# Kernel optimization log

Hardware: AMD Instinct MI355X
Metric: run time of the kernel (lower is better)

Reference implementation:

```python
import jax, jax.numpy as jnp
import numpy as np

B, L, H, NH = 4, 1024, 768, 12      # docs, seq len, hidden, attn heads
E, M, P = 30, 8, 512                # entities/doc, mentions/entity, ht pairs/doc
NLAB = 97                           # DocRED relation count
EMB, BLK = 768, 64                  # emb_size, block_size
OFFSET = 1                          # bert cls offset


def setup_inputs() -> dict:
    key = jax.random.key(0)
    ks = jax.random.split(key, 24)
    def n(k, shp, s=0.02):
        return jax.random.normal(k, shp, jnp.float32) * s
    seq_out = jax.random.normal(ks[0], (B, L, H), jnp.float32)
    attn = jax.random.uniform(ks[1], (B, NH, L, L), jnp.float32)
    mention_idx = jax.random.randint(ks[2], (B, E, M), 0, L - 2)
    ht_pairs = jax.random.randint(ks[3], (B, P, 2), 0, E)
    label_emb = jax.random.normal(ks[4], (NLAB, H), jnp.float32)
    adj = (jax.random.uniform(ks[5], (NLAB, NLAB)) < 0.2).astype(jnp.int32)
    label_adj = jnp.maximum(adj, jnp.eye(NLAB, dtype=jnp.int32))  # self loops
    return dict(
        seq_out=seq_out, attn=attn, mention_idx=mention_idx, ht_pairs=ht_pairs,
        label_adj=label_adj, label_emb=label_emb,
        gW0=n(ks[6], (H, 2 * 500)), gal0=n(ks[7], (2, 500)), gar0=n(ks[8], (2, 500)),
        gW1=n(ks[9], (1000, 2 * 500)), gal1=n(ks[10], (2, 500)), gar1=n(ks[11], (2, 500)),
        gW2=n(ks[12], (1000, H)), gal2=n(ks[13], (1, H)), gar2=n(ks[14], (1, H)),
        ln_gamma=jnp.ones((NLAB,), jnp.float32), ln_beta=jnp.zeros((NLAB,), jnp.float32),
        W_lin2=n(ks[15], (2 * NLAB, NLAB)), b_lin2=jnp.zeros((NLAB,), jnp.float32),
        W_head=n(ks[16], (2 * H, EMB)), b_head=jnp.zeros((EMB,), jnp.float32),
        W_tail=n(ks[17], (2 * H, EMB)), b_tail=jnp.zeros((EMB,), jnp.float32),
        W_bil=n(ks[18], (EMB * BLK + NLAB, NLAB)), b_bil=jnp.zeros((NLAB,), jnp.float32),
    )


def _gat_layer(x, W, al, ar, adj, act):
    nh, od = al.shape
    z = (x @ W).reshape(x.shape[0], nh, od)          # [N, nh, od]
    el = (z * al[None]).sum(-1)                      # src scores [N, nh]
    er = (z * ar[None]).sum(-1)                      # dst scores [N, nh]
    e = jax.nn.leaky_relu(er[:, None, :] + el[None, :, :], 0.2)  # [dst, src, nh]
    e = jnp.where((adj.T > 0)[:, :, None], e, -1e9)
    a = jax.nn.softmax(e, axis=1)
    out = jnp.einsum('vuh,uhd->vhd', a, z)
    return act(out) if act is not None else out


def _layer_norm(x, g, b, eps=1e-5):
    m = x.mean(-1, keepdims=True)
    v = ((x - m) ** 2).mean(-1, keepdims=True)
    return (x - m) * jax.lax.rsqrt(v + eps) * g + b


def _forward(seq_out, attn, label_emb, gW0, gal0, gar0, gW1, gal1, gar1,
             gW2, gal2, gar2, ln_gamma, ln_beta, W_lin2, b_lin2,
             W_head, b_head, W_tail, b_tail, W_bil, b_bil,
             mention_idx, ht_pairs, label_adj):
    pos = mention_idx + OFFSET                                   # [B,E,M]
    bidx3 = jnp.arange(B)[:, None, None]
    ment_emb = seq_out[bidx3, pos]                               # [B,E,M,H]
    ent_emb = jax.nn.logsumexp(ment_emb, axis=2)                 # [B,E,H]
    ment_att = attn[bidx3, :, pos]                               # [B,E,M,NH,L]
    ent_att = ment_att.mean(2)                                   # [B,E,NH,L]

    bidx2 = jnp.arange(B)[:, None]
    h_idx, t_idx = ht_pairs[..., 0], ht_pairs[..., 1]            # [B,P]
    hs = ent_emb[bidx2, h_idx]                                   # [B,P,H]
    ts = ent_emb[bidx2, t_idx]
    ht_att = (ent_att[bidx2, h_idx] * ent_att[bidx2, t_idx]).mean(2)  # [B,P,L]
    ht_att = ht_att / (ht_att.sum(-1, keepdims=True) + 1e-5)
    rs = jnp.einsum('bld,brl->brd', seq_out, ht_att)             # [B,P,H]

    N = B * P
    hs, ts, rs = hs.reshape(N, H), ts.reshape(N, H), rs.reshape(N, H)

    # label GAT: 2 hidden layers (2 heads, concat) + output head
    x = _gat_layer(label_emb, gW0, gal0, gar0, label_adj, None).reshape(NLAB, -1)
    x = jax.nn.elu(x)
    x = _gat_layer(x, gW1, gal1, gar1, label_adj, None).reshape(NLAB, -1)
    x = jax.nn.elu(x)
    lab = _gat_layer(x, gW2, gal2, gar2, label_adj, None).reshape(NLAB, H)

    hs_li = _layer_norm(hs @ lab.T, ln_gamma, ln_beta)           # [N,97]
    ts_li = _layer_norm(ts @ lab.T, ln_gamma, ln_beta)
    logits_li = jnp.concatenate([hs_li, ts_li], axis=1) @ W_lin2 + b_lin2

    hs2 = jnp.tanh(jnp.concatenate([hs, rs], axis=1) @ W_head + b_head)
    ts2 = jnp.tanh(jnp.concatenate([ts, rs], axis=1) @ W_tail + b_tail)
    b1 = hs2.reshape(N, EMB // BLK, BLK)
    b2 = ts2.reshape(N, EMB // BLK, BLK)
    bl = (b1[:, :, :, None] * b2[:, :, None, :]).reshape(N, EMB * BLK)
    logits = jnp.concatenate([bl, logits_li], axis=1) @ W_bil + b_bil
    return logits


def reference(seq_out, attn, mention_idx, ht_pairs, label_adj, label_emb,
              gW0, gal0, gar0, gW1, gal1, gar1, gW2, gal2, gar2,
              ln_gamma, ln_beta, W_lin2, b_lin2, W_head, b_head,
              W_tail, b_tail, W_bil, b_bil):
    return _forward(seq_out, attn, label_emb, gW0, gal0, gar0, gW1, gal1, gar1,
                    gW2, gal2, gar2, ln_gamma, ln_beta, W_lin2, b_lin2,
                    W_head, b_head, W_tail, b_tail, W_bil, b_bil,
                    mention_idx, ht_pairs, label_adj)
```

## Files before the change

kernel.cpp:

```cpp
#include <hip/hip_runtime.h>
#include <hip/hip_bf16.h>
#include <math.h>

typedef __hip_bfloat16 bf16;

__device__ __forceinline__ float toF(float x){ return x; }
__device__ __forceinline__ float toF(bf16 x){ return __bfloat162float(x); }
__device__ __forceinline__ void storeF(float v, float* p){ *p = v; }
__device__ __forceinline__ void storeF(float v, bf16* p){ *p = __float2bfloat16(v); }

__device__ __forceinline__ bool gateOff(const int* flag, int want){
    return flag && (*flag != want);
}

__global__ void detect_kernel(const unsigned int* gamma_bits, int* flag){
    if (threadIdx.x == 0) *flag = (gamma_bits[0] == 0x3F800000u) ? 0 : 1;
}

template<typename T>
__global__ void cvt_in(const T* __restrict__ in, float* __restrict__ out, int n,
                       const int* flag, int want){
    if (gateOff(flag, want)) return;
    int i = blockIdx.x*256 + threadIdx.x;
    if (i < n) out[i] = toF(in[i]);
}

template<typename T>
__global__ void store_out(const float* __restrict__ in, T* __restrict__ out, int n,
                          const int* flag, int want){
    if (gateOff(flag, want)) return;
    int i = blockIdx.x*256 + threadIdx.x;
    if (i < n) storeF(in[i], &out[i]);
}

template<typename T>
__global__ void ent_emb_kernel(const T* __restrict__ seq, const int* __restrict__ midx,
                               float* __restrict__ ent_emb, const int* flag, int want){
    if (gateOff(flag, want)) return;
    int be = blockIdx.x;
    int b  = be / 30;
    __shared__ int pos[8];
    if (threadIdx.x < 8) pos[threadIdx.x] = midx[be*8 + threadIdx.x] + 1;
    __syncthreads();
    for (int h = threadIdx.x; h < 768; h += 256){
        float v[8], mx = -1e30f;
        #pragma unroll
        for (int m=0;m<8;m++){
            v[m] = toF(seq[((size_t)b*1024 + pos[m])*768 + h]);
            mx = fmaxf(mx, v[m]);
        }
        float s = 0.f;
        #pragma unroll
        for (int m=0;m<8;m++) s += __expf(v[m]-mx);
        ent_emb[(size_t)be*768 + h] = mx + __logf(s);
    }
}

template<typename T>
__global__ void ent_att_kernel(const T* __restrict__ attn, const int* __restrict__ midx,
                               float* __restrict__ ent_att, const int* flag, int want){
    if (gateOff(flag, want)) return;
    int id = blockIdx.x;
    int nh = id % 12, be = id / 12, b = be / 30;
    __shared__ int pos[8];
    if (threadIdx.x < 8) pos[threadIdx.x] = midx[be*8 + threadIdx.x] + 1;
    __syncthreads();
    const size_t base = ((size_t)(b*12 + nh))*1024*1024;
    for (int l = threadIdx.x; l < 1024; l += 256){
        float s = 0.f;
        #pragma unroll
        for (int m=0;m<8;m++) s += toF(attn[base + (size_t)pos[m]*1024 + l]);
        ent_att[((size_t)be*12 + nh)*1024 + l] = s * 0.125f;
    }
}

__global__ void pair_kernel(const float* __restrict__ ent_emb, const float* __restrict__ ent_att,
                            const int* __restrict__ htp,
                            float* __restrict__ hs, float* __restrict__ ts, float* __restrict__ ht_att){
    int n = blockIdx.x;
    int b = n >> 9;
    int h = htp[n*2], t = htp[n*2+1];
    const float* eh = ent_emb + ((size_t)b*30 + h)*768;
    const float* et = ent_emb + ((size_t)b*30 + t)*768;
    for (int d = threadIdx.x; d < 768; d += 256){
        hs[(size_t)n*768 + d] = eh[d];
        ts[(size_t)n*768 + d] = et[d];
    }
    const float* ah = ent_att + ((size_t)b*30 + h)*12*1024;
    const float* at = ent_att + ((size_t)b*30 + t)*12*1024;
    float loc[4]; float psum = 0.f;
    #pragma unroll
    for (int i=0;i<4;i++){
        int l = threadIdx.x + i*256;
        float s = 0.f;
        #pragma unroll
        for (int k=0;k<12;k++) s += ah[k*1024 + l]*at[k*1024 + l];
        s *= (1.f/12.f);
        loc[i] = s; psum += s;
    }
    __shared__ float red[256];
    red[threadIdx.x] = psum; __syncthreads();
    for (int off=128; off>0; off>>=1){
        if (threadIdx.x < off) red[threadIdx.x] += red[threadIdx.x+off];
        __syncthreads();
    }
    float inv = 1.f/(red[0] + 1e-5f);
    #pragma unroll
    for (int i=0;i<4;i++){
        int l = threadIdx.x + i*256;
        ht_att[(size_t)n*1024 + l] = loc[i]*inv;
    }
}

template<typename T>
__global__ void rs_kernel(const T* __restrict__ seq, const float* __restrict__ ht_att,
                          float* __restrict__ rs, const int* flag, int want){
    if (gateOff(flag, want)) return;
    int hc = blockIdx.x;
    int pt = blockIdx.y;
    int b  = blockIdx.z;
    int h  = hc*256 + threadIdx.x;
    float acc[16];
    #pragma unroll
    for (int i=0;i<16;i++) acc[i]=0.f;
    __shared__ __align__(16) float att[64][20];
    for (int l0=0; l0<1024; l0+=64){
        for (int idx=threadIdx.x; idx<1024; idx+=256){
            int pl = idx>>6, lo = idx&63;
            att[lo][pl] = ht_att[((size_t)(b*512 + pt*16 + pl))*1024 + l0 + lo];
        }
        __syncthreads();
        for (int lo=0; lo<64; lo++){
            float sv = toF(seq[((size_t)b*1024 + l0 + lo)*768 + h]);
            #pragma unroll
            for (int p=0;p<16;p++) acc[p] += att[lo][p]*sv;
        }
        __syncthreads();
    }
    #pragma unroll
    for (int p=0;p<16;p++)
        rs[((size_t)(b*512 + pt*16 + p))*768 + h] = acc[p];
}

template<typename TB>
__global__ __launch_bounds__(256) void gemm64(const float* __restrict__ A1, const float* __restrict__ A2,
                                              int K1, int K, const TB* __restrict__ B,
                                              const TB* __restrict__ bias, int act,
                                              float* __restrict__ C, int M, int N,
                                              const int* flag, int want){
    if (gateOff(flag, want)) return;
    __shared__ __align__(16) float As[32][68];
    __shared__ __align__(16) float Bs[32][68];
    int m0 = blockIdx.y*64, n0 = blockIdx.x*64;
    int tid = threadIdx.x;
    int tr = tid>>4, tc = tid&15;
    float acc[4][4];
    #pragma unroll
    for (int i=0;i<4;i++)
        #pragma unroll
        for (int j=0;j<4;j++) acc[i][j]=0.f;
    int K2 = K - K1;
    for (int k0=0; k0<K; k0+=32){
        for (int e=tid; e<2048; e+=256){
            int k=e&31, m=e>>5;
            int gm=m0+m, gk=k0+k;
            float v=0.f;
            if (gm<M && gk<K) v = (gk<K1)? A1[(size_t)gm*K1+gk] : A2[(size_t)gm*K2 + (gk-K1)];
            As[k][m]=v;
        }
        for (int e=tid; e<2048; e+=256){
            int nn=e&63, k=e>>6;
            int gk=k0+k, gn=n0+nn;
            float v=0.f;
            if (gk<K && gn<N) v = toF(B[(size_t)gk*N+gn]);
            Bs[k][nn]=v;
        }
        __syncthreads();
        #pragma unroll
        for (int kk=0;kk<32;kk++){
            float4 a4 = *(const float4*)&As[kk][tr<<2];
            float4 b4 = *(const float4*)&Bs[kk][tc<<2];
            float av[4]={a4.x,a4.y,a4.z,a4.w}, bv[4]={b4.x,b4.y,b4.z,b4.w};
            #pragma unroll
            for (int i=0;i<4;i++)
                #pragma unroll
                for (int j=0;j<4;j++) acc[i][j] += av[i]*bv[j];
        }
        __syncthreads();
    }
    #pragma unroll
    for (int i=0;i<4;i++){
        int m = m0 + (tr<<2) + i;
        if (m >= M) continue;
        #pragma unroll
        for (int j=0;j<4;j++){
            int n = n0 + (tc<<2) + j;
            if (n >= N) continue;
            float v = acc[i][j];
            if (bias) v += toF(bias[n]);
            if (act == 1) v = tanhf(v);
            C[(size_t)m*N + n] = v;
        }
    }
}

template<typename T>
__global__ void elr_kernel(const float* __restrict__ z, const T* __restrict__ al,
                           const T* __restrict__ ar, int nh, int od,
                           float* __restrict__ el, float* __restrict__ er,
                           const int* flag, int want){
    if (gateOff(flag, want)) return;
    int u = blockIdx.x;
    __shared__ float sl[256], sr[256];
    int tid = threadIdx.x;
    for (int h=0; h<nh; h++){
        float a=0.f, r=0.f;
        for (int d=tid; d<od; d+=256){
            float zz = z[((size_t)u*nh + h)*od + d];
            a += zz*toF(al[h*od+d]);
            r += zz*toF(ar[h*od+d]);
        }
        sl[tid]=a; sr[tid]=r; __syncthreads();
        for (int off=128; off>0; off>>=1){
            if (tid<off){ sl[tid]+=sl[tid+off]; sr[tid]+=sr[tid+off]; }
            __syncthreads();
        }
        if (tid==0){ el[u*nh+h]=sl[0]; er[u*nh+h]=sr[0]; }
        __syncthreads();
    }
}

__global__ void gat_agg_kernel(const float* __restrict__ z, const float* __restrict__ el,
                               const float* __restrict__ er, const int* __restrict__ adj,
                               int nh, int od, int applyElu, float* __restrict__ out){
    int v = blockIdx.x;
    int tid = threadIdx.x;
    __shared__ float e[2][97];
    int D = nh*od;
    for (int idx=tid; idx<97*nh; idx+=256){
        int u = idx % 97, h = idx / 97;
        float ev;
        if (adj[u*97 + v] > 0){
            ev = er[v*nh+h] + el[u*nh+h];
            ev = ev > 0.f ? ev : 0.2f*ev;
        } else ev = -1e9f;
        e[h][u] = ev;
    }
    __syncthreads();
    if (tid < nh){
        float mx=-1e30f;
        for (int u2=0;u2<97;u2++) mx = fmaxf(mx, e[tid][u2]);
        float s=0.f;
        for (int u2=0;u2<97;u2++){ float x=__expf(e[tid][u2]-mx); e[tid][u2]=x; s+=x; }
        float inv = 1.f/s;
        for (int u2=0;u2<97;u2++) e[tid][u2]*=inv;
    }
    __syncthreads();
    for (int d0=tid; d0<D; d0+=256){
        int h = d0 / od;
        float s = 0.f;
        for (int u2=0;u2<97;u2++) s += e[h][u2]*z[(size_t)u2*D + d0];
        if (applyElu) s = s>0.f ? s : expm1f(s);
        out[(size_t)v*D + d0] = s;
    }
}

__global__ void transpose_kernel(const float* __restrict__ lab, float* __restrict__ labT){
    int i = blockIdx.x*256 + threadIdx.x;
    if (i < 97*768){ int c = i/768, k = i%768; labT[(size_t)k*97 + c] = lab[i]; }
}

template<typename T>
__global__ void ln_kernel(const float* __restrict__ in, const T* __restrict__ gamma,
                          const T* __restrict__ beta, float* __restrict__ out,
                          const int* flag, int want){
    if (gateOff(flag, want)) return;
    int n = blockIdx.x;
    int tid = threadIdx.x;
    __shared__ float red[128];
    float v = (tid < 97) ? in[(size_t)n*97 + tid] : 0.f;
    red[tid] = v; __syncthreads();
    for (int off=64; off>0; off>>=1){
        if (tid<off) red[tid]+=red[tid+off];
        __syncthreads();
    }
    float mean = red[0]*(1.f/97.f); __syncthreads();
    float d = (tid < 97) ? v - mean : 0.f;
    red[tid] = d*d; __syncthreads();
    for (int off=64; off>0; off>>=1){
        if (tid<off) red[tid]+=red[tid+off];
        __syncthreads();
    }
    float rstd = rsqrtf(red[0]*(1.f/97.f) + 1e-5f);
    if (tid < 97)
        out[(size_t)n*97 + tid] = d*rstd*toF(gamma[tid]) + toF(beta[tid]);
}

template<typename T>
__global__ __launch_bounds__(256) void bilinear_kernel(const float* __restrict__ hs2,
                                                       const float* __restrict__ ts2,
                                                       const T* __restrict__ Wb,
                                                       float* __restrict__ out,
                                                       const int* flag, int want){
    if (gateOff(flag, want)) return;
    int nb = blockIdx.x, g = blockIdx.y, ih = blockIdx.z;
    int n0 = nb*32;
    __shared__ __align__(16) float hsb[32][36];
    __shared__ __align__(16) float tsb[64][36];
    int tid = threadIdx.x;
    for (int e=tid; e<1024; e+=256){
        int i = e&31, nl = e>>5;
        hsb[i][nl] = hs2[(size_t)(n0+nl)*768 + g*64 + ih*32 + i];
    }
    for (int e=tid; e<2048; e+=256){
        int j = e&63, nl = e>>6;
        tsb[j][nl] = ts2[(size_t)(n0+nl)*768 + g*64 + j];
    }
    __syncthreads();
    int cg = tid & 63;
    int ng = tid >> 6;
    int c0 = cg, c1 = cg + 64;
    bool c1ok = (c1 < 97);
    const T* Wg = Wb + (size_t)g*4096*97 + (size_t)ih*32*64*97;
    float acc0[8], acc1[8];
    #pragma unroll
    for (int q=0;q<8;q++){ acc0[q]=0.f; acc1[q]=0.f; }
    for (int i=0;i<32;i++){
        float a[8];
        #pragma unroll
        for (int q=0;q<8;q++) a[q] = hsb[i][ng*8+q];
        const T* Wrow = Wg + (size_t)i*64*97;
        float s0[8], s1[8];
        #pragma unroll
        for (int q=0;q<8;q++){ s0[q]=0.f; s1[q]=0.f; }
        for (int j=0;j<64;j++){
            float w0 = toF(Wrow[(size_t)j*97 + c0]);
            float w1 = c1ok ? toF(Wrow[(size_t)j*97 + c1]) : 0.f;
            const float4* tp = (const float4*)&tsb[j][ng*8];
            float4 t0 = tp[0], t1 = tp[1];
            float tv[8] = {t0.x,t0.y,t0.z,t0.w,t1.x,t1.y,t1.z,t1.w};
            #pragma unroll
            for (int q=0;q<8;q++){ s0[q] += tv[q]*w0; s1[q] += tv[q]*w1; }
        }
        #pragma unroll
        for (int q=0;q<8;q++){ acc0[q] += a[q]*s0[q]; acc1[q] += a[q]*s1[q]; }
    }
    #pragma unroll
    for (int q=0;q<8;q++){
        int n = n0 + ng*8 + q;
        atomicAdd(&out[(size_t)n*97 + c0], acc0[q]);
        if (c1ok) atomicAdd(&out[(size_t)n*97 + c1], acc1[q]);
    }
}

extern "C" void kernel_launch(void* const* d_in, const int* in_sizes, int n_in,
                              void* d_out, int out_size, void* d_ws, size_t ws_size,
                              hipStream_t stream){
    (void)in_sizes; (void)n_in; (void)ws_size; (void)out_size;
    const void* seq   = d_in[0];
    const void* attn  = d_in[1];
    const int*  midx  = (const int*)d_in[2];
    const int*  htp   = (const int*)d_in[3];
    const int*  adj   = (const int*)d_in[4];
    const void* lemb  = d_in[5];
    const void* gW0   = d_in[6];
    const void* gal0  = d_in[7];
    const void* gar0  = d_in[8];
    const void* gW1   = d_in[9];
    const void* gal1  = d_in[10];
    const void* gar1  = d_in[11];
    const void* gW2   = d_in[12];
    const void* gal2  = d_in[13];
    const void* gar2  = d_in[14];
    const void* ln_g  = d_in[15];
    const void* ln_b  = d_in[16];
    const void* Wlin2 = d_in[17];
    const void* blin2 = d_in[18];
    const void* Whead = d_in[19];
    const void* bhead = d_in[20];
    const void* Wtail = d_in[21];
    const void* btail = d_in[22];
    const void* Wbil  = d_in[23];
    const void* bbil  = d_in[24];

    int*   flag = (int*)d_ws;
    float* base = (float*)d_ws + 16;
    float* hs     = base;
    float* ts     = hs + 1572864;
    float* R2     = ts + 1572864;
    float* ht_att = R2;
    float* hs2    = R2;
    float* li_raw = R2 + 1572864;
    float* R3     = R2 + 2097152;
    float* ent_emb= R3;
    float* ent_att= R3 + 92160;
    float* li     = R3;
    float* ts2    = R3;
    float* rs     = R3 + 1572864;
    float* sm     = rs + 1572864;
    float* x0   = sm;
    float* zbuf = x0 + 74496;
    float* x1   = zbuf + 97000;
    float* x2   = x1 + 97000;
    float* lab  = x2 + 97000;
    float* labT = lab + 74496;
    float* el   = labT + 74496;
    float* er   = el + 194;
    float* ll   = er + 194;
    float* logits = ll + 198656;

    detect_kernel<<<1,64,0,stream>>>((const unsigned int*)ln_g, flag);

    ent_emb_kernel<float><<<120,256,0,stream>>>((const float*)seq, midx, ent_emb, flag, 0);
    ent_emb_kernel<bf16 ><<<120,256,0,stream>>>((const bf16* )seq, midx, ent_emb, flag, 1);
    ent_att_kernel<float><<<1440,256,0,stream>>>((const float*)attn, midx, ent_att, flag, 0);
    ent_att_kernel<bf16 ><<<1440,256,0,stream>>>((const bf16* )attn, midx, ent_att, flag, 1);
    pair_kernel<<<2048,256,0,stream>>>(ent_emb, ent_att, htp, hs, ts, ht_att);
    rs_kernel<float><<<dim3(3,32,4),256,0,stream>>>((const float*)seq, ht_att, rs, flag, 0);
    rs_kernel<bf16 ><<<dim3(3,32,4),256,0,stream>>>((const bf16* )seq, ht_att, rs, flag, 1);

    cvt_in<float><<<(74496+255)/256,256,0,stream>>>((const float*)lemb, x0, 74496, flag, 0);
    cvt_in<bf16 ><<<(74496+255)/256,256,0,stream>>>((const bf16* )lemb, x0, 74496, flag, 1);

    auto gemm_pair = [&](const float* A1, const float* A2, int K1, int K,
                         const void* B, const void* bias, int act,
                         float* C, int M, int N, dim3 grid){
        gemm64<float><<<grid,256,0,stream>>>(A1,A2,K1,K,(const float*)B,(const float*)bias,act,C,M,N,flag,0);
        gemm64<bf16 ><<<grid,256,0,stream>>>(A1,A2,K1,K,(const bf16* )B,(const bf16* )bias,act,C,M,N,flag,1);
    };
    auto elr_pair = [&](const float* z, const void* al, const void* ar, int nh, int od){
        elr_kernel<float><<<97,256,0,stream>>>(z,(const float*)al,(const float*)ar,nh,od,el,er,flag,0);
        elr_kernel<bf16 ><<<97,256,0,stream>>>(z,(const bf16* )al,(const bf16* )ar,nh,od,el,er,flag,1);
    };

    gemm_pair(x0, nullptr, 768, 768, gW0, nullptr, 0, zbuf, 97, 1000, dim3(16,2));
    elr_pair(zbuf, gal0, gar0, 2, 500);
    gat_agg_kernel<<<97,256,0,stream>>>(zbuf, el, er, adj, 2, 500, 1, x1);
    gemm_pair(x1, nullptr, 1000, 1000, gW1, nullptr, 0, zbuf, 97, 1000, dim3(16,2));
    elr_pair(zbuf, gal1, gar1, 2, 500);
    gat_agg_kernel<<<97,256,0,stream>>>(zbuf, el, er, adj, 2, 500, 1, x2);
    gemm_pair(x2, nullptr, 1000, 1000, gW2, nullptr, 0, zbuf, 97, 768, dim3(12,2));
    elr_pair(zbuf, gal2, gar2, 1, 768);
    gat_agg_kernel<<<97,256,0,stream>>>(zbuf, el, er, adj, 1, 768, 0, lab);
    transpose_kernel<<<(74496+255)/256,256,0,stream>>>(lab, labT);

    gemm64<float><<<dim3(2,64),256,0,stream>>>(hs, nullptr, 768, 768, labT,
        (const float*)nullptr, 0, li_raw, 4096, 97, nullptr, 0);
    ln_kernel<float><<<4096,128,0,stream>>>(li_raw, (const float*)ln_g, (const float*)ln_b, li, flag, 0);
    ln_kernel<bf16 ><<<4096,128,0,stream>>>(li_raw, (const bf16* )ln_g, (const bf16* )ln_b, li, flag, 1);
    gemm_pair(li, li + 2048*97, 97, 194, Wlin2, blin2, 0, ll, 2048, 97, dim3(2,32));

    gemm_pair(hs, rs, 768, 1536, Whead, bhead, 1, hs2, 2048, 768, dim3(12,32));
    gemm_pair(ts, rs, 768, 1536, Wtail, btail, 1, ts2, 2048, 768, dim3(12,32));

    gemm64<float><<<dim3(2,32),256,0,stream>>>(ll, nullptr, 97, 97,
        (const float*)Wbil + (size_t)49152*97, (const float*)bbil, 0, logits, 2048, 97, flag, 0);
    gemm64<bf16 ><<<dim3(2,32),256,0,stream>>>(ll, nullptr, 97, 97,
        (const bf16* )Wbil + (size_t)49152*97, (const bf16* )bbil, 0, logits, 2048, 97, flag, 1);

    bilinear_kernel<float><<<dim3(64,12,2),256,0,stream>>>(hs2, ts2, (const float*)Wbil, logits, flag, 0);
    bilinear_kernel<bf16 ><<<dim3(64,12,2),256,0,stream>>>(hs2, ts2, (const bf16* )Wbil, logits, flag, 1);

    store_out<float><<<(198656+255)/256,256,0,stream>>>(logits, (float*)d_out, 198656, flag, 0);
    store_out<bf16 ><<<(198656+255)/256,256,0,stream>>>(logits, (bf16*)d_out, 198656, flag, 1);
}
```

Baseline: 2.677 ms.

## Double-buffer bilinear weight rows through LDS with register prefetch

The bilinear kernel now stages each 64x97 weight slice in shared memory through a two-buffer scheme. The next slice is prefetched into registers while the current one is consumed, and bf16 weights are unpacked with bit shifts. Before this, each thread read the weights directly from global memory with strided scalar loads. The change adds about 50KB of LDS per block plus extra registers and a barrier per iteration, which may reduce occupancy.

```diff
diff --git a/kernel.cpp b/kernel.cpp
--- a/kernel.cpp
+++ b/kernel.cpp
@@ -8,6 +8,9 @@
 __device__ __forceinline__ float toF(bf16 x){ return __bfloat162float(x); }
 __device__ __forceinline__ void storeF(float v, float* p){ *p = v; }
 __device__ __forceinline__ void storeF(float v, bf16* p){ *p = __float2bfloat16(v); }
+
+__device__ __forceinline__ float bfLo(unsigned u){ return __uint_as_float(u << 16); }
+__device__ __forceinline__ float bfHi(unsigned u){ return __uint_as_float(u & 0xFFFF0000u); }
 
 __device__ __forceinline__ bool gateOff(const int* flag, int want){
     return flag && (*flag != want);
@@ -307,6 +310,7 @@
     int n0 = nb*32;
     __shared__ __align__(16) float hsb[32][36];
     __shared__ __align__(16) float tsb[64][36];
+    __shared__ __align__(16) float w_lds[2][6208];
     int tid = threadIdx.x;
     for (int e=tid; e<1024; e+=256){
         int i = e&31, nl = e>>5;
@@ -316,26 +320,61 @@
         int j = e&63, nl = e>>6;
         tsb[j][nl] = ts2[(size_t)(n0+nl)*768 + g*64 + j];
     }
+    const T* Wg = Wb + (size_t)g*4096*97 + (size_t)ih*32*6208;
+
+    if constexpr (sizeof(T) == 4){
+        const float4* src = (const float4*)Wg;
+        float4* dst = (float4*)w_lds[0];
+        #pragma unroll
+        for (int u=0;u<7;u++){ int e = tid + u*256; if (e < 1552) dst[e] = src[e]; }
+    } else {
+        const uint4* src = (const uint4*)Wg;
+        #pragma unroll
+        for (int u=0;u<4;u++){
+            int e = tid + u*256;
+            if (e < 776){
+                uint4 w = src[e];
+                float* d = &w_lds[0][e*8];
+                d[0]=bfLo(w.x); d[1]=bfHi(w.x); d[2]=bfLo(w.y); d[3]=bfHi(w.y);
+                d[4]=bfLo(w.z); d[5]=bfHi(w.z); d[6]=bfLo(w.w); d[7]=bfHi(w.w);
+            }
+        }
+    }
     __syncthreads();
+
     int cg = tid & 63;
     int ng = tid >> 6;
     int c0 = cg, c1 = cg + 64;
     bool c1ok = (c1 < 97);
-    const T* Wg = Wb + (size_t)g*4096*97 + (size_t)ih*32*64*97;
     float acc0[8], acc1[8];
     #pragma unroll
     for (int q=0;q<8;q++){ acc0[q]=0.f; acc1[q]=0.f; }
+
+    int cur = 0;
     for (int i=0;i<32;i++){
+        float4 wreg[7];
+        uint4  breg[4];
+        if (i+1 < 32){
+            if constexpr (sizeof(T) == 4){
+                const float4* src = (const float4*)(Wg + (size_t)(i+1)*6208);
+                #pragma unroll
+                for (int u=0;u<7;u++){ int e = tid + u*256; if (e < 1552) wreg[u] = src[e]; }
+            } else {
+                const uint4* src = (const uint4*)(Wg + (size_t)(i+1)*6208);
+                #pragma unroll
+                for (int u=0;u<4;u++){ int e = tid + u*256; if (e < 776) breg[u] = src[e]; }
+            }
+        }
         float a[8];
         #pragma unroll
         for (int q=0;q<8;q++) a[q] = hsb[i][ng*8+q];
-        const T* Wrow = Wg + (size_t)i*64*97;
         float s0[8], s1[8];
         #pragma unroll
         for (int q=0;q<8;q++){ s0[q]=0.f; s1[q]=0.f; }
+        const float* wrow = w_lds[cur];
         for (int j=0;j<64;j++){
-            float w0 = toF(Wrow[(size_t)j*97 + c0]);
-            float w1 = c1ok ? toF(Wrow[(size_t)j*97 + c1]) : 0.f;
+            float w0 = wrow[j*97 + c0];
+            float w1 = c1ok ? wrow[j*97 + c1] : 0.f;
             const float4* tp = (const float4*)&tsb[j][ng*8];
             float4 t0 = tp[0], t1 = tp[1];
             float tv[8] = {t0.x,t0.y,t0.z,t0.w,t1.x,t1.y,t1.z,t1.w};
@@ -344,6 +383,27 @@
         }
         #pragma unroll
         for (int q=0;q<8;q++){ acc0[q] += a[q]*s0[q]; acc1[q] += a[q]*s1[q]; }
+        if (i+1 < 32){
+            if constexpr (sizeof(T) == 4){
+                float4* dst = (float4*)w_lds[cur^1];
+                #pragma unroll
+                for (int u=0;u<7;u++){ int e = tid + u*256; if (e < 1552) dst[e] = wreg[u]; }
+            } else {
+                float* base = w_lds[cur^1];
+                #pragma unroll
+                for (int u=0;u<4;u++){
+                    int e = tid + u*256;
+                    if (e < 776){
+                        uint4 w = breg[u];
+                        float* d = &base[e*8];
+                        d[0]=bfLo(w.x); d[1]=bfHi(w.x); d[2]=bfLo(w.y); d[3]=bfHi(w.y);
+                        d[4]=bfLo(w.z); d[5]=bfHi(w.z); d[6]=bfLo(w.w); d[7]=bfHi(w.w);
+                    }
+                }
+            }
+        }
+        __syncthreads();
+        cur ^= 1;
     }
     #pragma unroll
     for (int q=0;q<8;q++){
```

Result: slower. 2.784 ms (+4.0%).
